# Kernel optimization log

Hardware: AMD Instinct MI355X
Metric: run time of the kernel (lower is better)

## Reference

```python
import jax, jax.numpy as jnp
import numpy as np

B, D_IN, D_H = 1024, 4096, 4096


def setup_inputs() -> dict:
    key = jax.random.key(0)
    ks = jax.random.split(key, 11)
    s_i = 1.0 / np.sqrt(0.5 * (D_IN + D_H))  # xavier_normal std for i2h
    s_h = 1.0 / np.sqrt(D_H)                 # xavier_normal std for h2h
    inp = {
        "x": jax.random.normal(ks[0], (B, D_IN), jnp.float32),
        "h_prev": jax.random.normal(ks[1], (B, D_H), jnp.float32),
        "c_prev": jax.random.normal(ks[2], (B, D_H), jnp.float32),
        "Wi": jax.random.normal(ks[3], (D_IN, D_H), jnp.float32) * s_i,
        "Ui": jax.random.normal(ks[4], (D_H, D_H), jnp.float32) * s_h,
        "bi": jnp.zeros((D_H,), jnp.float32),
        "Wf": jax.random.normal(ks[5], (D_IN, D_H), jnp.float32) * s_i,
        "Uf": jax.random.normal(ks[6], (D_H, D_H), jnp.float32) * s_h,
        "bf": jnp.zeros((D_H,), jnp.float32),
        "Wg": jax.random.normal(ks[7], (D_IN, D_H), jnp.float32) * s_i,
        "Ug": jax.random.normal(ks[8], (D_H, D_H), jnp.float32) * s_h,
        "bg": jnp.zeros((D_H,), jnp.float32),
        "Wo": jax.random.normal(ks[9], (D_IN, D_H), jnp.float32) * s_i,
        "Uo": jax.random.normal(ks[10], (D_H, D_H), jnp.float32) * s_h,
        "bo": jnp.zeros((D_H,), jnp.float32),
    }
    return inp


def reference(x, h_prev, c_prev, Wi, Ui, bi, Wf, Uf, bf, Wg, Ug, bg, Wo, Uo, bo):
    # Fuse the 8 small GEMMs into 2 by concatenating weights along the output dim.
    W = jnp.concatenate([Wi, Wf, Wg, Wo], axis=1)   # [D_IN, 4*D_H]
    U = jnp.concatenate([Ui, Uf, Ug, Uo], axis=1)   # [D_H, 4*D_H]
    b = jnp.concatenate([bi, bf, bg, bo], axis=0)   # [4*D_H]
    z = x @ W + h_prev @ U + b                      # [B, 4*D_H]
    zi, zf, zg, zo = jnp.split(z, 4, axis=1)
    ig = jax.nn.sigmoid(zi)
    fg = jax.nn.sigmoid(zf)
    cc = jnp.tanh(zg)
    og = jax.nn.sigmoid(zo)
    c = fg * c_prev + ig * cc
    h = og * jnp.tanh(c)
    return (h, c)
```

## Files before the change

kernel.cpp:

```cpp
#include <hip/hip_runtime.h>
#include <cstdint>
#include <cstddef>


typedef __bf16 bf16;
typedef __bf16 bf16x8 __attribute__((ext_vector_type(8)));
typedef __bf16 bf16x4 __attribute__((ext_vector_type(4)));
typedef float f32x4 __attribute__((ext_vector_type(4)));

static constexpr int Bn = 1024;
static constexpr int DH = 4096;
static constexpr int K  = 8192;
static constexpr int BM = 512, BN = 64, BK = 32;

__device__ __forceinline__ void load_lds16(const void* g, void* l) {
  __builtin_amdgcn_global_load_lds(
      (const __attribute__((address_space(1))) unsigned int*)g,
      (__attribute__((address_space(3))) unsigned int*)l, 16, 0, 0);
}

__global__ void pack_A(const float* __restrict__ x, const float* __restrict__ h,
                       bf16* __restrict__ A) {
  int idx4 = blockIdx.x * blockDim.x + threadIdx.x;
  int b = idx4 >> 11;
  int q = idx4 & 2047;
  int k = q << 2;
  const float* src = (k < DH) ? (x + (size_t)b * DH + k)
                              : (h + (size_t)b * DH + (k - DH));
  float4 v = *(const float4*)src;
  bf16x4 o;
  o[0] = (bf16)v.x; o[1] = (bf16)v.y; o[2] = (bf16)v.z; o[3] = (bf16)v.w;
  *(bf16x4*)(A + (size_t)idx4 * 4) = o;
}

__global__ __launch_bounds__(256) void conv_w2(
    const float* __restrict__ Wi, const float* __restrict__ Ui,
    const float* __restrict__ Wf, const float* __restrict__ Uf,
    const float* __restrict__ Wg, const float* __restrict__ Ug,
    const float* __restrict__ Wo, const float* __restrict__ Uo,
    bf16* __restrict__ Bt) {
  __shared__ short tile[64 * 256];
  const int bz = blockIdx.z;
  const int gate = bz >> 1, isU = bz & 1;
  const float* src;
  switch (bz) {
    case 0: src = Wi; break; case 1: src = Ui; break;
    case 2: src = Wf; break; case 3: src = Uf; break;
    case 4: src = Wg; break; case 5: src = Ug; break;
    default: src = (bz == 6) ? Wo : Uo; break;
  }
  const int k0 = blockIdx.x * 256, n0 = blockIdx.y * 64;
  const int t = threadIdx.x;
  const int c = t & 15;
  const int pr = t >> 4;
#pragma unroll
  for (int it = 0; it < 8; ++it) {
    const int R = it * 16 + pr;
    const int k = 2 * R;
    float4 v0 = *(const float4*)(src + (size_t)(k0 + k) * DH + n0 + c * 4);
    float4 v1 = *(const float4*)(src + (size_t)(k0 + k + 1) * DH + n0 + c * 4);
    const int chunk = R >> 2, sub = R & 3;
#pragma unroll
    for (int i = 0; i < 4; ++i) {
      const int nl = c * 4 + i;
      bf16 lo = (bf16)((&v0.x)[i]);
      bf16 hi = (bf16)((&v1.x)[i]);
      short2 pk;
      pk.x = __builtin_bit_cast(short, lo);
      pk.y = __builtin_bit_cast(short, hi);
      *(short2*)&tile[nl * 256 + ((chunk ^ (nl & 7)) << 3) + (sub << 1)] = pk;
    }
  }
  __syncthreads();
  const int u = t & 31;
#pragma unroll
  for (int rr = 0; rr < 8; ++rr) {
    const int nl = rr * 8 + (t >> 5);
    bf16x8 val = *(const bf16x8*)&tile[nl * 256 + ((u ^ (nl & 7)) << 3)];
    const int hc = n0 + nl;
    const size_t row = (size_t)((hc >> 4) * 64 + gate * 16 + (hc & 15));
    *(bf16x8*)(Bt + row * K + (size_t)(isU * DH + k0 + 8 * u)) = val;
  }
}

__device__ __forceinline__ float sigm(float x) { return 1.0f / (1.0f + __expf(-x)); }
__device__ __forceinline__ float tanh_(float x) { return 1.0f - 2.0f / (__expf(2.0f * x) + 1.0f); }

__global__ __launch_bounds__(256, 2) void lstm_gemm(
    const bf16* __restrict__ A, const bf16* __restrict__ Bt,
    const float* __restrict__ cp,
    const float* __restrict__ bi, const float* __restrict__ bfv,
    const float* __restrict__ bg, const float* __restrict__ bo,
    float* __restrict__ out) {
  __shared__ __align__(16) bf16 As[BM * BK];
  __shared__ __align__(16) bf16 Bs[BN * BK];
  const int m0 = blockIdx.x * BM;
  const int n0 = blockIdx.y * BN;
  const int t = threadIdx.x, l = t & 63, w = t >> 6;
  const int lane15 = l & 15, quad = l >> 4;
  const int srow = l >> 2;
  const int skk = (l & 3) * 8;

  f32x4 acc[8][4];
#pragma unroll
  for (int i = 0; i < 8; ++i)
#pragma unroll
    for (int j = 0; j < 4; ++j) acc[i][j] = (f32x4)0.0f;

  for (int kt = 0; kt < K / BK; ++kt) {
    const int k0 = kt * BK;
#pragma unroll
    for (int cc = 0; cc < 8; ++cc) {
      const int row = m0 + w * 128 + cc * 16 + srow;
      load_lds16(A + (size_t)row * K + k0 + skk, (char*)As + (w * 8 + cc) * 1024);
    }
    load_lds16(Bt + (size_t)(n0 + w * 16 + srow) * K + k0 + skk, (char*)Bs + w * 1024);
    __syncthreads();
    bf16x8 aF[8], bF[4];
#pragma unroll
    for (int i = 0; i < 8; ++i)
      aF[i] = *(const bf16x8*)(As + (w * 128 + i * 16 + lane15) * BK + quad * 8);
#pragma unroll
    for (int j = 0; j < 4; ++j)
      bF[j] = *(const bf16x8*)(Bs + (j * 16 + lane15) * BK + quad * 8);
#pragma unroll
    for (int i = 0; i < 8; ++i)
#pragma unroll
      for (int j = 0; j < 4; ++j)
        acc[i][j] = __builtin_amdgcn_mfma_f32_16x16x32_bf16(aF[i], bF[j], acc[i][j], 0, 0, 0);
    __syncthreads();
  }

  const int hc = blockIdx.y * 16 + lane15;
  const float vbi = bi[hc], vbf = bfv[hc], vbg = bg[hc], vbo = bo[hc];
  float* outh = out;
  float* outc = out + (size_t)Bn * DH;
#pragma unroll
  for (int i = 0; i < 8; ++i) {
    const int brow = m0 + w * 128 + i * 16 + quad * 4;
#pragma unroll
    for (int r = 0; r < 4; ++r) {
      const int b = brow + r;
      const float zi = acc[i][0][r] + vbi;
      const float zf = acc[i][1][r] + vbf;
      const float zg = acc[i][2][r] + vbg;
      const float zo = acc[i][3][r] + vbo;
      const float ig = sigm(zi), fg = sigm(zf), gg = tanh_(zg), og = sigm(zo);
      const float cprev = cp[(size_t)b * DH + hc];
      const float cnew = fg * cprev + ig * gg;
      outh[(size_t)b * DH + hc] = og * tanh_(cnew);
      outc[(size_t)b * DH + hc] = cnew;
    }
  }
}

extern "C" void kernel_launch(void* const* d_in, const int* in_sizes, int n_in,
                              void* d_out, int out_size, void* d_ws, size_t ws_size,
                              hipStream_t stream) {
  const float* x  = (const float*)d_in[0];
  const float* hp = (const float*)d_in[1];
  const float* cp = (const float*)d_in[2];
  const float* Wi = (const float*)d_in[3];
  const float* Ui = (const float*)d_in[4];
  const float* bi = (const float*)d_in[5];
  const float* Wf = (const float*)d_in[6];
  const float* Uf = (const float*)d_in[7];
  const float* bf = (const float*)d_in[8];
  const float* Wg = (const float*)d_in[9];
  const float* Ug = (const float*)d_in[10];
  const float* bg = (const float*)d_in[11];
  const float* Wo = (const float*)d_in[12];
  const float* Uo = (const float*)d_in[13];
  const float* bo = (const float*)d_in[14];

  bf16* Aw = (bf16*)d_ws;
  bf16* Bt = (bf16*)((char*)d_ws + ((size_t)16 << 20));

  hipLaunchKernelGGL(conv_w2, dim3(16, 64, 8), dim3(256), 0, stream,
                     Wi, Ui, Wf, Uf, Wg, Ug, Wo, Uo, Bt);
  hipLaunchKernelGGL(pack_A, dim3((Bn * K / 4) / 256), dim3(256), 0, stream, x, hp, Aw);
  hipLaunchKernelGGL(lstm_gemm, dim3(Bn / BM, (4 * DH) / BN), dim3(256), 0, stream,
                     Aw, Bt, cp, bi, bf, bg, bo, (float*)d_out);
}
```

Measured before the change: 919.1 us.

## Rework weight transpose tiling, swap GEMM grid order, and change LDS fragment layout

The weight conversion kernel now transposes through a padded fp32 LDS tile in four 64-row K slices, converting to bf16 on the read side instead of packing into a swizzled bf16 tile. The GEMM grid is swapped so the N dimension is blockIdx.x, which changes which blocks run together and how A and B tiles are reused in cache. The LDS layout for A and B fragments becomes quad-major (lane15 contiguous), so each lane's global-to-LDS load matches the MFMA fragment read pattern. The aim is fewer LDS bank conflicts and better L2 locality, at the cost of more syncthreads in the transpose kernel.

After: 1.143 ms. 1.24x slower.

```diff
diff --git a/kernel.cpp b/kernel.cpp
--- a/kernel.cpp
+++ b/kernel.cpp
@@ -33,13 +33,13 @@
   *(bf16x4*)(A + (size_t)idx4 * 4) = o;
 }
 
-__global__ __launch_bounds__(256) void conv_w2(
+__global__ __launch_bounds__(256) void conv_w3(
     const float* __restrict__ Wi, const float* __restrict__ Ui,
     const float* __restrict__ Wf, const float* __restrict__ Uf,
     const float* __restrict__ Wg, const float* __restrict__ Ug,
     const float* __restrict__ Wo, const float* __restrict__ Uo,
     bf16* __restrict__ Bt) {
-  __shared__ short tile[64 * 256];
+  __shared__ float tile[64 * 65];
   const int bz = blockIdx.z;
   const int gate = bz >> 1, isU = bz & 1;
   const float* src;
@@ -51,35 +51,34 @@
   }
   const int k0 = blockIdx.x * 256, n0 = blockIdx.y * 64;
   const int t = threadIdx.x;
-  const int c = t & 15;
-  const int pr = t >> 4;
+  const int c  = t & 15;
+  const int kr = t >> 4;
+  const int n2 = t >> 3;
+  const int u  = t & 7;
+
+  for (int s = 0; s < 4; ++s) {
+    const int ks = k0 + s * 64;
 #pragma unroll
-  for (int it = 0; it < 8; ++it) {
-    const int R = it * 16 + pr;
-    const int k = 2 * R;
-    float4 v0 = *(const float4*)(src + (size_t)(k0 + k) * DH + n0 + c * 4);
-    float4 v1 = *(const float4*)(src + (size_t)(k0 + k + 1) * DH + n0 + c * 4);
-    const int chunk = R >> 2, sub = R & 3;
+    for (int ii = 0; ii < 4; ++ii) {
+      const int kk = ii * 16 + kr;
+      float4 v = *(const float4*)(src + (size_t)(ks + kk) * DH + n0 + c * 4);
+      const float* vp = &v.x;
 #pragma unroll
-    for (int i = 0; i < 4; ++i) {
-      const int nl = c * 4 + i;
-      bf16 lo = (bf16)((&v0.x)[i]);
-      bf16 hi = (bf16)((&v1.x)[i]);
-      short2 pk;
-      pk.x = __builtin_bit_cast(short, lo);
-      pk.y = __builtin_bit_cast(short, hi);
-      *(short2*)&tile[nl * 256 + ((chunk ^ (nl & 7)) << 3) + (sub << 1)] = pk;
+      for (int j = 0; j < 4; ++j) tile[(c * 4 + j) * 65 + kk] = vp[j];
     }
-  }
-  __syncthreads();
-  const int u = t & 31;
+    __syncthreads();
 #pragma unroll
-  for (int rr = 0; rr < 8; ++rr) {
-    const int nl = rr * 8 + (t >> 5);
-    bf16x8 val = *(const bf16x8*)&tile[nl * 256 + ((u ^ (nl & 7)) << 3)];
-    const int hc = n0 + nl;
-    const size_t row = (size_t)((hc >> 4) * 64 + gate * 16 + (hc & 15));
-    *(bf16x8*)(Bt + row * K + (size_t)(isU * DH + k0 + 8 * u)) = val;
+    for (int jj = 0; jj < 2; ++jj) {
+      const int nl = jj * 32 + n2;
+      const float* p = &tile[nl * 65 + u * 8];
+      bf16x8 o;
+#pragma unroll
+      for (int e = 0; e < 8; ++e) o[e] = (bf16)p[e];
+      const int hc = n0 + nl;
+      const size_t row = (size_t)((hc >> 4) * 64 + gate * 16 + (hc & 15));
+      *(bf16x8*)(Bt + row * K + (size_t)(isU * DH + ks + 8 * u)) = o;
+    }
+    __syncthreads();
   }
 }
 
@@ -94,12 +93,10 @@
     float* __restrict__ out) {
   __shared__ __align__(16) bf16 As[BM * BK];
   __shared__ __align__(16) bf16 Bs[BN * BK];
-  const int m0 = blockIdx.x * BM;
-  const int n0 = blockIdx.y * BN;
+  const int n0 = blockIdx.x * BN;
+  const int m0 = blockIdx.y * BM;
   const int t = threadIdx.x, l = t & 63, w = t >> 6;
   const int lane15 = l & 15, quad = l >> 4;
-  const int srow = l >> 2;
-  const int skk = (l & 3) * 8;
 
   f32x4 acc[8][4];
 #pragma unroll
@@ -111,18 +108,22 @@
     const int k0 = kt * BK;
 #pragma unroll
     for (int cc = 0; cc < 8; ++cc) {
-      const int row = m0 + w * 128 + cc * 16 + srow;
-      load_lds16(A + (size_t)row * K + k0 + skk, (char*)As + (w * 8 + cc) * 1024);
+      const int bb = w * 8 + cc;
+      load_lds16(A + (size_t)(m0 + bb * 16 + lane15) * K + k0 + quad * 8,
+                 (char*)As + bb * 1024);
     }
-    load_lds16(Bt + (size_t)(n0 + w * 16 + srow) * K + k0 + skk, (char*)Bs + w * 1024);
+    load_lds16(Bt + (size_t)(n0 + w * 16 + lane15) * K + k0 + quad * 8,
+               (char*)Bs + w * 1024);
     __syncthreads();
     bf16x8 aF[8], bF[4];
 #pragma unroll
     for (int i = 0; i < 8; ++i)
-      aF[i] = *(const bf16x8*)(As + (w * 128 + i * 16 + lane15) * BK + quad * 8);
+      aF[i] = *(const bf16x8*)((const char*)As + ((w * 8 + i) << 10) +
+                               (quad << 8) + (lane15 << 4));
 #pragma unroll
     for (int j = 0; j < 4; ++j)
-      bF[j] = *(const bf16x8*)(Bs + (j * 16 + lane15) * BK + quad * 8);
+      bF[j] = *(const bf16x8*)((const char*)Bs + (j << 10) +
+                               (quad << 8) + (lane15 << 4));
 #pragma unroll
     for (int i = 0; i < 8; ++i)
 #pragma unroll
@@ -131,7 +132,7 @@
     __syncthreads();
   }
 
-  const int hc = blockIdx.y * 16 + lane15;
+  const int hc = blockIdx.x * 16 + lane15;
   const float vbi = bi[hc], vbf = bfv[hc], vbg = bg[hc], vbo = bo[hc];
   float* outh = out;
   float* outc = out + (size_t)Bn * DH;
@@ -176,9 +177,9 @@
   bf16* Aw = (bf16*)d_ws;
   bf16* Bt = (bf16*)((char*)d_ws + ((size_t)16 << 20));
 
-  hipLaunchKernelGGL(conv_w2, dim3(16, 64, 8), dim3(256), 0, stream,
+  hipLaunchKernelGGL(conv_w3, dim3(16, 64, 8), dim3(256), 0, stream,
                      Wi, Ui, Wf, Uf, Wg, Ug, Wo, Uo, Bt);
   hipLaunchKernelGGL(pack_A, dim3((Bn * K / 4) / 256), dim3(256), 0, stream, x, hp, Aw);
-  hipLaunchKernelGGL(lstm_gemm, dim3(Bn / BM, (4 * DH) / BN), dim3(256), 0, stream,
+  hipLaunchKernelGGL(lstm_gemm, dim3((4 * DH) / BN, Bn / BM), dim3(256), 0, stream,
                      Aw, Bt, cp, bi, bf, bg, bo, (float*)d_out);
 }
```
